# Performance work log

Measured on AMD Instinct MI355X. Metric: run time of the kernel, lower is better.

Reference implementation:

```python
import jax, jax.numpy as jnp
import numpy as np

DIM = 512
HID = 1024
E = 8          # num_experts
K = 2          # num_experts_per_tok
B, S = 4, 2048


def setup_inputs() -> dict:
    key = jax.random.key(0)
    ks = jax.random.split(key, 10)
    sd = DIM ** -0.5
    sh = HID ** -0.5
    return {
        "x": jax.random.normal(ks[0], (B, S, DIM), dtype=jnp.float32),
        "gate_w": jax.random.normal(ks[1], (E, DIM), dtype=jnp.float32) * sd,
        "biases": jnp.zeros((E,), dtype=jnp.float32),  # e_expert_biases
        # routed experts: swiglu  y = (silu(x@w1) * (x@w3)) @ w2
        "w1": jax.random.normal(ks[2], (E, DIM, HID), dtype=jnp.float32) * sd,
        "w3": jax.random.normal(ks[3], (E, DIM, HID), dtype=jnp.float32) * sd,
        "w2": jax.random.normal(ks[4], (E, HID, DIM), dtype=jnp.float32) * sh,
        # single shared expert
        "sw1": jax.random.normal(ks[5], (DIM, HID), dtype=jnp.float32) * sd,
        "sw3": jax.random.normal(ks[6], (DIM, HID), dtype=jnp.float32) * sd,
        "sw2": jax.random.normal(ks[7], (HID, DIM), dtype=jnp.float32) * sh,
    }


def reference(x, gate_w, biases, w1, w3, w2, sw1, sw3, sw2):
    Bb, Ss, D = x.shape
    xt = x.reshape(Bb * Ss, D)                      # [T, D]

    # shared expert (applied to full x)
    shared = (jax.nn.silu(xt @ sw1) * (xt @ sw3)) @ sw2  # [T, D]

    # router
    scores = xt @ gate_w.T                          # [T, E]
    # indices chosen from biased scores (aux-free load balancing)
    _, idx = jax.lax.top_k(scores + biases, K)      # [T, K] int
    # gate values are top-k of the UNBIASED scores (as in original code)
    topv, _ = jax.lax.top_k(scores, K)              # [T, K]
    p = jax.nn.sigmoid(topv)
    p = p / jnp.sum(p, axis=-1, keepdims=True)      # [T, K]

    # every expert on every token (dense-combine MoE reference)
    h = jax.nn.silu(jnp.einsum('td,edh->eth', xt, w1)) * jnp.einsum('td,edh->eth', xt, w3)
    y = jnp.einsum('eth,ehd->etd', h, w2)           # [E, T, D]

    onehot = jax.nn.one_hot(idx, E, dtype=xt.dtype)  # [T, K, E]
    comb = jnp.einsum('tk,tke->te', p, onehot)       # [T, E] combine weights
    out = jnp.einsum('te,etd->td', comb, y) + shared
    return out.reshape(Bb, Ss, D)
```

## Files before the change

### kernel.cpp

```cpp
#include <hip/hip_runtime.h>
#include <hip/hip_bf16.h>


#define Tn 8192
#define Dd 512
#define Hh 1024
#define NEx 9

typedef __attribute__((ext_vector_type(8))) short short8;
typedef __attribute__((ext_vector_type(4))) float f32x4;

#define AS1 __attribute__((address_space(1)))
#define AS3 __attribute__((address_space(3)))

#define OFF_XB    ((size_t)0)
#define OFF_W1T   (OFF_XB + (size_t)Tn * Dd * 2)
#define OFF_W3T   (OFF_W1T + (size_t)NEx * Hh * Dd * 2)
#define OFF_W2T   (OFF_W3T + (size_t)NEx * Hh * Dd * 2)
#define OFF_HBUF  (OFF_W2T + (size_t)NEx * Dd * Hh * 2)
#define OFF_TOK   (OFF_HBUF + (size_t)(3 * Tn) * Hh * 2)
#define OFF_SLOTP (OFF_TOK + (size_t)8 * Tn * 4)
#define OFF_PG    (OFF_SLOTP + (size_t)Tn * 2 * 4)
#define OFF_CNT   (OFF_PG + (size_t)Tn * 2 * 4)
#define OFF_OFFS  (OFF_CNT + 1024)
#define OFF_YC    OFF_XB

__device__ __forceinline__ ushort f2bf(float f) {
    unsigned int u = __float_as_uint(f);
    return (ushort)((u + 0x7fffu + ((u >> 16) & 1u)) >> 16);
}
__device__ __forceinline__ float bf2f(short s) {
    return __uint_as_float(((unsigned int)(unsigned short)s) << 16);
}

__global__ __launch_bounds__(256) void trans_kernel(
        const float* __restrict__ w1, const float* __restrict__ sw1,
        const float* __restrict__ w3, const float* __restrict__ sw3,
        const float* __restrict__ w2, const float* __restrict__ sw2,
        ushort* __restrict__ w1t, ushort* __restrict__ w3t, ushort* __restrict__ w2t) {
    __shared__ float tile[32][33];
    int z = blockIdx.z;
    int fam = z / 9, sl = z - fam * 9;
    const float* src; ushort* dst;
    int R, C, r0, c0;
    if (fam == 0)      { src = (sl < 8) ? w1 + (size_t)sl * Dd * Hh : sw1; dst = w1t + (size_t)sl * Dd * Hh; R = Dd; C = Hh; c0 = blockIdx.x * 32; r0 = blockIdx.y * 32; }
    else if (fam == 1) { src = (sl < 8) ? w3 + (size_t)sl * Dd * Hh : sw3; dst = w3t + (size_t)sl * Dd * Hh; R = Dd; C = Hh; c0 = blockIdx.x * 32; r0 = blockIdx.y * 32; }
    else               { src = (sl < 8) ? w2 + (size_t)sl * Dd * Hh : sw2; dst = w2t + (size_t)sl * Dd * Hh; R = Hh; C = Dd; r0 = blockIdx.x * 32; c0 = blockIdx.y * 32; }
    int tx = threadIdx.x & 31, ty = threadIdx.x >> 5;
#pragma unroll
    for (int k = 0; k < 4; ++k)
        tile[ty + 8 * k][tx] = src[(size_t)(r0 + ty + 8 * k) * C + c0 + tx];
    __syncthreads();
#pragma unroll
    for (int k = 0; k < 4; ++k)
        dst[(size_t)(c0 + ty + 8 * k) * R + r0 + tx] = f2bf(tile[tx][ty + 8 * k]);
}

__global__ __launch_bounds__(256) void router_kernel(const float* __restrict__ x,
                                                     const float* __restrict__ gw,
                                                     const float* __restrict__ bias,
                                                     int* __restrict__ cnt,
                                                     int* __restrict__ tok,
                                                     int* __restrict__ slotp,
                                                     float* __restrict__ pg,
                                                     ushort* __restrict__ xb) {
    __shared__ int le[64];
    __shared__ float lg[64];
    __shared__ int lpos[64];
    __shared__ int lcnt[8];
    __shared__ int gbase[8];
    int tid = threadIdx.x, lane = tid & 63, wave = tid >> 6;
    if (tid < 8) lcnt[tid] = 0;
    __syncthreads();
    int t0 = blockIdx.x * 32 + wave * 8;
    for (int it = 0; it < 8; ++it) {
        int t = t0 + it;
        const float4* xr = (const float4*)(x + (size_t)t * Dd);
        float4 xa = xr[lane * 2], xc = xr[lane * 2 + 1];
        ushort4 o1, o2;
        o1.x = f2bf(xa.x); o1.y = f2bf(xa.y); o1.z = f2bf(xa.z); o1.w = f2bf(xa.w);
        o2.x = f2bf(xc.x); o2.y = f2bf(xc.y); o2.z = f2bf(xc.z); o2.w = f2bf(xc.w);
        *(ushort4*)(xb + (size_t)t * Dd + lane * 8) = o1;
        *(ushort4*)(xb + (size_t)t * Dd + lane * 8 + 4) = o2;
        float sc[8];
#pragma unroll
        for (int e = 0; e < 8; ++e) {
            const float4* gr = (const float4*)(gw + (size_t)e * Dd);
            float4 ga = gr[lane * 2], gc = gr[lane * 2 + 1];
            float s = xa.x * ga.x + xa.y * ga.y + xa.z * ga.z + xa.w * ga.w
                    + xc.x * gc.x + xc.y * gc.y + xc.z * gc.z + xc.w * gc.w;
#pragma unroll
            for (int o = 32; o > 0; o >>= 1) s += __shfl_xor(s, o);
            sc[e] = s;
        }
        if (lane == 0) {
            float b0 = -1e30f; int i0 = 0;
#pragma unroll
            for (int e = 0; e < 8; ++e) { float bv = sc[e] + bias[e]; if (bv > b0) { b0 = bv; i0 = e; } }
            float b1v = -1e30f; int i1 = (i0 == 0) ? 1 : 0;
#pragma unroll
            for (int e = 0; e < 8; ++e) if (e != i0) { float bv = sc[e] + bias[e]; if (bv > b1v) { b1v = bv; i1 = e; } }
            float v0 = -1e30f; int k0i = 0;
#pragma unroll
            for (int e = 0; e < 8; ++e) if (sc[e] > v0) { v0 = sc[e]; k0i = e; }
            float v1 = -1e30f;
#pragma unroll
            for (int e = 0; e < 8; ++e) if (e != k0i && sc[e] > v1) v1 = sc[e];
            float p0 = 1.f / (1.f + __expf(-v0));
            float p1 = 1.f / (1.f + __expf(-v1));
            float inv = 1.f / (p0 + p1);
            int ai = (wave * 8 + it) * 2;
            le[ai] = i0;     lg[ai] = p0 * inv;
            le[ai + 1] = i1; lg[ai + 1] = p1 * inv;
        }
    }
    __syncthreads();
    if (tid < 64) lpos[tid] = atomicAdd(&lcnt[le[tid]], 1);
    __syncthreads();
    if (tid < 8) gbase[tid] = atomicAdd(&cnt[tid * 32], lcnt[tid]);
    __syncthreads();
    if (tid < 64) {
        int e = le[tid];
        int dst = gbase[e] + lpos[tid];
        int t = blockIdx.x * 32 + (tid >> 1);
        tok[(size_t)e * Tn + dst] = t;
        slotp[t * 2 + (tid & 1)] = (e << 16) | dst;
        pg[t * 2 + (tid & 1)] = lg[tid];
    }
}

__global__ void scan_kernel(const int* cnt, int* off, int* cntc) {
    if (threadIdx.x == 0 && blockIdx.x == 0) {
        int s = 0;
        for (int e = 0; e < 8; ++e) { int c = cnt[e * 32]; cntc[e] = c; off[e] = s; s += c; }
        off[8] = s;
        cntc[8] = Tn;
    }
}

__global__ __launch_bounds__(256, 2) void stage1_kernel(
        const ushort* __restrict__ xb, const ushort* __restrict__ w1t,
        const ushort* __restrict__ w3t, const int* __restrict__ tok,
        const int* __restrict__ cntc, const int* __restrict__ off,
        ushort* __restrict__ Hbuf) {
    int e = blockIdx.z;
    int cn = cntc[e];
    int m0 = blockIdx.x * 128;
    if (m0 >= cn) return;
    int n0 = blockIdx.y * 128;
    const ushort* w1e = w1t + (size_t)e * Hh * Dd;
    const ushort* w3e = w3t + (size_t)e * Hh * Dd;

    __shared__ ushort As[128 * 64];
    __shared__ ushort B1s[128 * 64];
    __shared__ ushort B3s[128 * 64];
    __shared__ int toks[128];

    int tid = threadIdx.x;
    if (tid < 128) {
        int slot = m0 + tid;
        int sl = slot < cn ? slot : cn - 1;
        toks[tid] = (e == 8) ? sl : tok[(size_t)e * Tn + sl];
    }
    __syncthreads();

    int lane = tid & 63, wave = tid >> 6;
    int wm = (wave & 1) * 64, wn = (wave >> 1) * 64;
    int col15 = lane & 15, quad = lane >> 4;
    int lr = lane >> 3;
    int lcx = ((lane & 7) ^ lr) * 8;

    f32x4 acc1[4][4], acc3[4][4];
#pragma unroll
    for (int a = 0; a < 4; ++a)
#pragma unroll
        for (int b = 0; b < 4; ++b) {
            acc1[a][b] = (f32x4){0.f, 0.f, 0.f, 0.f};
            acc3[a][b] = (f32x4){0.f, 0.f, 0.f, 0.f};
        }

    for (int kb = 0; kb < Dd; kb += 64) {
#pragma unroll
        for (int i = 0; i < 4; ++i) {
            int cid = wave * 4 + i;
            const ushort* g = xb + (size_t)toks[cid * 8 + lr] * Dd + kb + lcx;
            __builtin_amdgcn_global_load_lds((const AS1 void*)g, (AS3 void*)(As + cid * 512), 16, 0, 0);
        }
#pragma unroll
        for (int i = 0; i < 4; ++i) {
            int cid = wave * 4 + i;
            int r = n0 + cid * 8 + lr;
            const ushort* g1 = w1e + (size_t)r * Dd + kb + lcx;
            const ushort* g3 = w3e + (size_t)r * Dd + kb + lcx;
            __builtin_amdgcn_global_load_lds((const AS1 void*)g1, (AS3 void*)(B1s + cid * 512), 16, 0, 0);
            __builtin_amdgcn_global_load_lds((const AS1 void*)g3, (AS3 void*)(B3s + cid * 512), 16, 0, 0);
        }
        __syncthreads();
#pragma unroll
        for (int ks = 0; ks < 2; ++ks) {
            int px = ((ks * 4 + quad) ^ (col15 & 7)) * 8;
            short8 a[4], b1[4], b3[4];
#pragma unroll
            for (int mi = 0; mi < 4; ++mi)
                a[mi] = *(const short8*)&As[(wm + mi * 16 + col15) * 64 + px];
#pragma unroll
            for (int ni = 0; ni < 4; ++ni) {
                b1[ni] = *(const short8*)&B1s[(wn + ni * 16 + col15) * 64 + px];
                b3[ni] = *(const short8*)&B3s[(wn + ni * 16 + col15) * 64 + px];
            }
#pragma unroll
            for (int mi = 0; mi < 4; ++mi)
#pragma unroll
                for (int ni = 0; ni < 4; ++ni) {
                    acc1[mi][ni] = __builtin_amdgcn_mfma_f32_16x16x32_bf16(a[mi], b1[ni], acc1[mi][ni], 0, 0, 0);
                    acc3[mi][ni] = __builtin_amdgcn_mfma_f32_16x16x32_bf16(a[mi], b3[ni], acc3[mi][ni], 0, 0, 0);
                }
        }
        __syncthreads();
    }

    int oe = off[e];
#pragma unroll
    for (int mi = 0; mi < 4; ++mi)
#pragma unroll
        for (int r = 0; r < 4; ++r) {
            int slot = m0 + wm + mi * 16 + quad * 4 + r;
            if (slot < cn) {
                size_t rowb = (size_t)(oe + slot) * Hh;
#pragma unroll
                for (int ni = 0; ni < 4; ++ni) {
                    float h1 = acc1[mi][ni][r], h3 = acc3[mi][ni][r];
                    float s = h1 / (1.f + __expf(-h1));
                    Hbuf[rowb + n0 + wn + ni * 16 + col15] = f2bf(s * h3);
                }
            }
        }
}

__global__ __launch_bounds__(256, 3) void stage2_kernel(
        const ushort* __restrict__ Hbuf, const ushort* __restrict__ w2t,
        const int* __restrict__ cntc, const int* __restrict__ off,
        ushort* __restrict__ Yc) {
    int e = blockIdx.z;
    int cn = cntc[e];
    int m0 = blockIdx.x * 128;
    if (m0 >= cn) return;
    int n0 = blockIdx.y * 128;
    int oe = off[e];
    const ushort* w2e = w2t + (size_t)e * Dd * Hh;

    __shared__ ushort As[128 * 64];
    __shared__ ushort Bs[128 * 64];

    int tid = threadIdx.x;
    int lane = tid & 63, wave = tid >> 6;
    int wm = (wave & 1) * 64, wn = (wave >> 1) * 64;
    int col15 = lane & 15, quad = lane >> 4;
    int lr = lane >> 3;
    int lcx = ((lane & 7) ^ lr) * 8;

    f32x4 acc[4][4];
#pragma unroll
    for (int a = 0; a < 4; ++a)
#pragma unroll
        for (int b = 0; b < 4; ++b) acc[a][b] = (f32x4){0.f, 0.f, 0.f, 0.f};

    for (int kb = 0; kb < Hh; kb += 64) {
#pragma unroll
        for (int i = 0; i < 4; ++i) {
            int cid = wave * 4 + i;
            const ushort* g = Hbuf + (size_t)(oe + m0 + cid * 8 + lr) * Hh + kb + lcx;
            __builtin_amdgcn_global_load_lds((const AS1 void*)g, (AS3 void*)(As + cid * 512), 16, 0, 0);
        }
#pragma unroll
        for (int i = 0; i < 4; ++i) {
            int cid = wave * 4 + i;
            const ushort* g = w2e + (size_t)(n0 + cid * 8 + lr) * Hh + kb + lcx;
            __builtin_amdgcn_global_load_lds((const AS1 void*)g, (AS3 void*)(Bs + cid * 512), 16, 0, 0);
        }
        __syncthreads();
#pragma unroll
        for (int ks = 0; ks < 2; ++ks) {
            int px = ((ks * 4 + quad) ^ (col15 & 7)) * 8;
            short8 a[4], b[4];
#pragma unroll
            for (int mi = 0; mi < 4; ++mi)
                a[mi] = *(const short8*)&As[(wm + mi * 16 + col15) * 64 + px];
#pragma unroll
            for (int ni = 0; ni < 4; ++ni)
                b[ni] = *(const short8*)&Bs[(wn + ni * 16 + col15) * 64 + px];
#pragma unroll
            for (int mi = 0; mi < 4; ++mi)
#pragma unroll
                for (int ni = 0; ni < 4; ++ni)
                    acc[mi][ni] = __builtin_amdgcn_mfma_f32_16x16x32_bf16(a[mi], b[ni], acc[mi][ni], 0, 0, 0);
        }
        __syncthreads();
    }

#pragma unroll
    for (int mi = 0; mi < 4; ++mi)
#pragma unroll
        for (int r = 0; r < 4; ++r) {
            int slot = m0 + wm + mi * 16 + quad * 4 + r;
            if (slot < cn) {
                size_t rowb = (size_t)(oe + slot) * Dd;
#pragma unroll
                for (int ni = 0; ni < 4; ++ni)
                    Yc[rowb + n0 + wn + ni * 16 + col15] = f2bf(acc[mi][ni][r]);
            }
        }
}

__global__ __launch_bounds__(256) void combine_kernel(const ushort* __restrict__ Yc,
        const int* __restrict__ slotp, const float* __restrict__ pg,
        const int* __restrict__ off, float* __restrict__ out) {
    int g = blockIdx.x * 256 + threadIdx.x;
    int t = g >> 6;
    int c = (g & 63) * 8;
    int p0 = slotp[t * 2], p1 = slotp[t * 2 + 1];
    float g0 = pg[t * 2], g1 = pg[t * 2 + 1];
    int s0 = off[p0 >> 16] + (p0 & 0xffff);
    int s1 = off[p1 >> 16] + (p1 & 0xffff);
    int s2 = off[8] + t;
    short8 a = *(const short8*)(Yc + (size_t)s0 * Dd + c);
    short8 b = *(const short8*)(Yc + (size_t)s1 * Dd + c);
    short8 d = *(const short8*)(Yc + (size_t)s2 * Dd + c);
    float o[8];
#pragma unroll
    for (int i = 0; i < 8; ++i)
        o[i] = g0 * bf2f(a[i]) + g1 * bf2f(b[i]) + bf2f(d[i]);
    float* dst = out + (size_t)t * Dd + c;
    *(float4*)dst = (float4){o[0], o[1], o[2], o[3]};
    *(float4*)(dst + 4) = (float4){o[4], o[5], o[6], o[7]};
}

extern "C" void kernel_launch(void* const* d_in, const int* in_sizes, int n_in,
                              void* d_out, int out_size, void* d_ws, size_t ws_size,
                              hipStream_t stream) {
    (void)in_sizes; (void)n_in; (void)out_size; (void)ws_size;
    const float* x    = (const float*)d_in[0];
    const float* gw   = (const float*)d_in[1];
    const float* bias = (const float*)d_in[2];
    const float* w1   = (const float*)d_in[3];
    const float* w3   = (const float*)d_in[4];
    const float* w2   = (const float*)d_in[5];
    const float* sw1  = (const float*)d_in[6];
    const float* sw3  = (const float*)d_in[7];
    const float* sw2  = (const float*)d_in[8];
    float* out = (float*)d_out;

    char* ws = (char*)d_ws;
    ushort* xb    = (ushort*)(ws + OFF_XB);
    ushort* w1t   = (ushort*)(ws + OFF_W1T);
    ushort* w3t   = (ushort*)(ws + OFF_W3T);
    ushort* w2t   = (ushort*)(ws + OFF_W2T);
    ushort* Hbuf  = (ushort*)(ws + OFF_HBUF);
    ushort* Yc    = (ushort*)(ws + OFF_YC);
    int*    tok   = (int*)(ws + OFF_TOK);
    int*    slotp = (int*)(ws + OFF_SLOTP);
    float*  pg    = (float*)(ws + OFF_PG);
    int*    cnt   = (int*)(ws + OFF_CNT);
    int*    off   = (int*)(ws + OFF_OFFS);
    int*    cntc  = off + 16;

    hipMemsetAsync(cnt, 0, 1024, stream);

    trans_kernel<<<dim3(32, 16, 27), 256, 0, stream>>>(w1, sw1, w3, sw3, w2, sw2, w1t, w3t, w2t);
    router_kernel<<<256, 256, 0, stream>>>(x, gw, bias, cnt, tok, slotp, pg, xb);
    scan_kernel<<<1, 64, 0, stream>>>(cnt, off, cntc);

    stage1_kernel<<<dim3(64, Hh / 128, NEx), 256, 0, stream>>>(xb, w1t, w3t, tok, cntc, off, Hbuf);
    stage2_kernel<<<dim3(64, Dd / 128, NEx), 256, 0, stream>>>(Hbuf, w2t, cntc, off, Yc);
    combine_kernel<<<2048, 256, 0, stream>>>(Yc, slotp, pg, off, out);
}
```

Baseline: 278.3 us.

## Interleave w1/w3 weights into one matrix to halve stage1 tile accumulators

The transpose kernel now writes w1 and w3 into one interleaved [2H, D] bf16 matrix, alternating in 16-row blocks. Stage1 then loads a single B tile and keeps one set of accumulators instead of two, pairing adjacent 16-column fragments for the SwiGLU epilogue. The grid doubles along N to cover 2H. This cuts per-block registers and LDS use, which should allow more occupancy, but the A tile is now reloaded by twice as many blocks.

```diff
diff --git a/kernel.cpp b/kernel.cpp
--- a/kernel.cpp
+++ b/kernel.cpp
@@ -14,9 +14,8 @@
 #define AS3 __attribute__((address_space(3)))
 
 #define OFF_XB    ((size_t)0)
-#define OFF_W1T   (OFF_XB + (size_t)Tn * Dd * 2)
-#define OFF_W3T   (OFF_W1T + (size_t)NEx * Hh * Dd * 2)
-#define OFF_W2T   (OFF_W3T + (size_t)NEx * Hh * Dd * 2)
+#define OFF_W13T  (OFF_XB + (size_t)Tn * Dd * 2)
+#define OFF_W2T   (OFF_W13T + (size_t)NEx * 2 * Hh * Dd * 2)
 #define OFF_HBUF  (OFF_W2T + (size_t)NEx * Dd * Hh * 2)
 #define OFF_TOK   (OFF_HBUF + (size_t)(3 * Tn) * Hh * 2)
 #define OFF_SLOTP (OFF_TOK + (size_t)8 * Tn * 4)
@@ -37,23 +36,38 @@
         const float* __restrict__ w1, const float* __restrict__ sw1,
         const float* __restrict__ w3, const float* __restrict__ sw3,
         const float* __restrict__ w2, const float* __restrict__ sw2,
-        ushort* __restrict__ w1t, ushort* __restrict__ w3t, ushort* __restrict__ w2t) {
+        ushort* __restrict__ w13t, ushort* __restrict__ w2t) {
     __shared__ float tile[32][33];
     int z = blockIdx.z;
     int fam = z / 9, sl = z - fam * 9;
-    const float* src; ushort* dst;
-    int R, C, r0, c0;
-    if (fam == 0)      { src = (sl < 8) ? w1 + (size_t)sl * Dd * Hh : sw1; dst = w1t + (size_t)sl * Dd * Hh; R = Dd; C = Hh; c0 = blockIdx.x * 32; r0 = blockIdx.y * 32; }
-    else if (fam == 1) { src = (sl < 8) ? w3 + (size_t)sl * Dd * Hh : sw3; dst = w3t + (size_t)sl * Dd * Hh; R = Dd; C = Hh; c0 = blockIdx.x * 32; r0 = blockIdx.y * 32; }
-    else               { src = (sl < 8) ? w2 + (size_t)sl * Dd * Hh : sw2; dst = w2t + (size_t)sl * Dd * Hh; R = Hh; C = Dd; r0 = blockIdx.x * 32; c0 = blockIdx.y * 32; }
     int tx = threadIdx.x & 31, ty = threadIdx.x >> 5;
-#pragma unroll
-    for (int k = 0; k < 4; ++k)
-        tile[ty + 8 * k][tx] = src[(size_t)(r0 + ty + 8 * k) * C + c0 + tx];
-    __syncthreads();
-#pragma unroll
-    for (int k = 0; k < 4; ++k)
-        dst[(size_t)(c0 + ty + 8 * k) * R + r0 + tx] = f2bf(tile[tx][ty + 8 * k]);
+    if (fam < 2) {
+        const float* base = (fam == 0) ? ((sl < 8) ? w1 + (size_t)sl * Dd * Hh : sw1)
+                                       : ((sl < 8) ? w3 + (size_t)sl * Dd * Hh : sw3);
+        ushort* dst = w13t + (size_t)sl * 2 * Hh * Dd;
+        int c0 = blockIdx.x * 32, r0 = blockIdx.y * 32;
+#pragma unroll
+        for (int k = 0; k < 4; ++k)
+            tile[ty + 8 * k][tx] = base[(size_t)(r0 + ty + 8 * k) * Hh + c0 + tx];
+        __syncthreads();
+#pragma unroll
+        for (int k = 0; k < 4; ++k) {
+            int h = c0 + ty + 8 * k;
+            int n = (((h >> 4) * 2 + fam) << 4) + (h & 15);
+            dst[(size_t)n * Dd + r0 + tx] = f2bf(tile[tx][ty + 8 * k]);
+        }
+    } else {
+        const float* base = (sl < 8) ? w2 + (size_t)sl * Dd * Hh : sw2;
+        ushort* dst = w2t + (size_t)sl * Dd * Hh;
+        int r0 = blockIdx.x * 32, c0 = blockIdx.y * 32;
+#pragma unroll
+        for (int k = 0; k < 4; ++k)
+            tile[ty + 8 * k][tx] = base[(size_t)(r0 + ty + 8 * k) * Dd + c0 + tx];
+        __syncthreads();
+#pragma unroll
+        for (int k = 0; k < 4; ++k)
+            dst[(size_t)(c0 + ty + 8 * k) * Hh + r0 + tx] = f2bf(tile[tx][ty + 8 * k]);
+    }
 }
 
 __global__ __launch_bounds__(256) void router_kernel(const float* __restrict__ x,
@@ -139,21 +153,18 @@
 }
 
 __global__ __launch_bounds__(256, 2) void stage1_kernel(
-        const ushort* __restrict__ xb, const ushort* __restrict__ w1t,
-        const ushort* __restrict__ w3t, const int* __restrict__ tok,
-        const int* __restrict__ cntc, const int* __restrict__ off,
-        ushort* __restrict__ Hbuf) {
+        const ushort* __restrict__ xb, const ushort* __restrict__ w13t,
+        const int* __restrict__ tok, const int* __restrict__ cntc,
+        const int* __restrict__ off, ushort* __restrict__ Hbuf) {
     int e = blockIdx.z;
     int cn = cntc[e];
     int m0 = blockIdx.x * 128;
     if (m0 >= cn) return;
     int n0 = blockIdx.y * 128;
-    const ushort* w1e = w1t + (size_t)e * Hh * Dd;
-    const ushort* w3e = w3t + (size_t)e * Hh * Dd;
+    const ushort* we = w13t + (size_t)e * 2 * Hh * Dd;
 
     __shared__ ushort As[128 * 64];
-    __shared__ ushort B1s[128 * 64];
-    __shared__ ushort B3s[128 * 64];
+    __shared__ ushort Bs[128 * 64];
     __shared__ int toks[128];
 
     int tid = threadIdx.x;
@@ -170,14 +181,11 @@
     int lr = lane >> 3;
     int lcx = ((lane & 7) ^ lr) * 8;
 
-    f32x4 acc1[4][4], acc3[4][4];
+    f32x4 acc[4][4];
 #pragma unroll
     for (int a = 0; a < 4; ++a)
 #pragma unroll
-        for (int b = 0; b < 4; ++b) {
-            acc1[a][b] = (f32x4){0.f, 0.f, 0.f, 0.f};
-            acc3[a][b] = (f32x4){0.f, 0.f, 0.f, 0.f};
-        }
+        for (int b = 0; b < 4; ++b) acc[a][b] = (f32x4){0.f, 0.f, 0.f, 0.f};
 
     for (int kb = 0; kb < Dd; kb += 64) {
 #pragma unroll
@@ -189,37 +197,31 @@
 #pragma unroll
         for (int i = 0; i < 4; ++i) {
             int cid = wave * 4 + i;
-            int r = n0 + cid * 8 + lr;
-            const ushort* g1 = w1e + (size_t)r * Dd + kb + lcx;
-            const ushort* g3 = w3e + (size_t)r * Dd + kb + lcx;
-            __builtin_amdgcn_global_load_lds((const AS1 void*)g1, (AS3 void*)(B1s + cid * 512), 16, 0, 0);
-            __builtin_amdgcn_global_load_lds((const AS1 void*)g3, (AS3 void*)(B3s + cid * 512), 16, 0, 0);
+            const ushort* g = we + (size_t)(n0 + cid * 8 + lr) * Dd + kb + lcx;
+            __builtin_amdgcn_global_load_lds((const AS1 void*)g, (AS3 void*)(Bs + cid * 512), 16, 0, 0);
         }
         __syncthreads();
 #pragma unroll
         for (int ks = 0; ks < 2; ++ks) {
             int px = ((ks * 4 + quad) ^ (col15 & 7)) * 8;
-            short8 a[4], b1[4], b3[4];
+            short8 a[4], b[4];
 #pragma unroll
             for (int mi = 0; mi < 4; ++mi)
                 a[mi] = *(const short8*)&As[(wm + mi * 16 + col15) * 64 + px];
 #pragma unroll
-            for (int ni = 0; ni < 4; ++ni) {
-                b1[ni] = *(const short8*)&B1s[(wn + ni * 16 + col15) * 64 + px];
-                b3[ni] = *(const short8*)&B3s[(wn + ni * 16 + col15) * 64 + px];
-            }
+            for (int ni = 0; ni < 4; ++ni)
+                b[ni] = *(const short8*)&Bs[(wn + ni * 16 + col15) * 64 + px];
 #pragma unroll
             for (int mi = 0; mi < 4; ++mi)
 #pragma unroll
-                for (int ni = 0; ni < 4; ++ni) {
-                    acc1[mi][ni] = __builtin_amdgcn_mfma_f32_16x16x32_bf16(a[mi], b1[ni], acc1[mi][ni], 0, 0, 0);
-                    acc3[mi][ni] = __builtin_amdgcn_mfma_f32_16x16x32_bf16(a[mi], b3[ni], acc3[mi][ni], 0, 0, 0);
-                }
+                for (int ni = 0; ni < 4; ++ni)
+                    acc[mi][ni] = __builtin_amdgcn_mfma_f32_16x16x32_bf16(a[mi], b[ni], acc[mi][ni], 0, 0, 0);
         }
         __syncthreads();
     }
 
     int oe = off[e];
+    int hbase = (n0 + wn) >> 1;
 #pragma unroll
     for (int mi = 0; mi < 4; ++mi)
 #pragma unroll
@@ -228,10 +230,10 @@
             if (slot < cn) {
                 size_t rowb = (size_t)(oe + slot) * Hh;
 #pragma unroll
-                for (int ni = 0; ni < 4; ++ni) {
-                    float h1 = acc1[mi][ni][r], h3 = acc3[mi][ni][r];
+                for (int np = 0; np < 2; ++np) {
+                    float h1 = acc[mi][np * 2][r], h3 = acc[mi][np * 2 + 1][r];
                     float s = h1 / (1.f + __expf(-h1));
-                    Hbuf[rowb + n0 + wn + ni * 16 + col15] = f2bf(s * h3);
+                    Hbuf[rowb + hbase + np * 16 + col15] = f2bf(s * h3);
                 }
             }
         }
@@ -352,8 +354,7 @@
 
     char* ws = (char*)d_ws;
     ushort* xb    = (ushort*)(ws + OFF_XB);
-    ushort* w1t   = (ushort*)(ws + OFF_W1T);
-    ushort* w3t   = (ushort*)(ws + OFF_W3T);
+    ushort* w13t  = (ushort*)(ws + OFF_W13T);
     ushort* w2t   = (ushort*)(ws + OFF_W2T);
     ushort* Hbuf  = (ushort*)(ws + OFF_HBUF);
     ushort* Yc    = (ushort*)(ws + OFF_YC);
@@ -366,11 +367,11 @@
 
     hipMemsetAsync(cnt, 0, 1024, stream);
 
-    trans_kernel<<<dim3(32, 16, 27), 256, 0, stream>>>(w1, sw1, w3, sw3, w2, sw2, w1t, w3t, w2t);
+    trans_kernel<<<dim3(32, 16, 27), 256, 0, stream>>>(w1, sw1, w3, sw3, w2, sw2, w13t, w2t);
     router_kernel<<<256, 256, 0, stream>>>(x, gw, bias, cnt, tok, slotp, pg, xb);
     scan_kernel<<<1, 64, 0, stream>>>(cnt, off, cntc);
 
-    stage1_kernel<<<dim3(64, Hh / 128, NEx), 256, 0, stream>>>(xb, w1t, w3t, tok, cntc, off, Hbuf);
+    stage1_kernel<<<dim3(64, 16, NEx), 256, 0, stream>>>(xb, w13t, tok, cntc, off, Hbuf);
     stage2_kernel<<<dim3(64, Dd / 128, NEx), 256, 0, stream>>>(Hbuf, w2t, cntc, off, Yc);
     combine_kernel<<<2048, 256, 0, stream>>>(Yc, slotp, pg, off, out);
 }
```

Measured after the change: 263.0 us. 5.5% less time.
